# Optimization experiments

Measured on AMD Instinct MI355X. Metric: run time of the kernel, lower is better.

## Reference

```python
import jax, jax.numpy as jnp
import numpy as np
import math

DIM = 1024
NUM_HEADS = 16
HEAD_DIM = DIM // NUM_HEADS
MAX_SEQ_LEN = 2048


def setup_inputs() -> dict:
    key = jax.random.key(0)
    ks = jax.random.split(key, 10)
    B, S = 4, 2048
    std = 1.0 / math.sqrt(DIM)
    inp = {
        "x": jax.random.normal(ks[0], (B, S, DIM), dtype=jnp.float32),
        "key_padding_mask": jnp.zeros((B, S), dtype=jnp.bool_),
        "q_w": jax.random.uniform(ks[1], (DIM, DIM), minval=-std, maxval=std),
        "q_b": jax.random.uniform(ks[2], (DIM,), minval=-std, maxval=std),
        "k_w": jax.random.uniform(ks[3], (DIM, DIM), minval=-std, maxval=std),
        "k_b": jax.random.uniform(ks[4], (DIM,), minval=-std, maxval=std),
        "v_w": jax.random.uniform(ks[5], (DIM, DIM), minval=-std, maxval=std),
        "v_b": jax.random.uniform(ks[6], (DIM,), minval=-std, maxval=std),
        "o_w": jax.random.uniform(ks[7], (DIM, DIM), minval=-std, maxval=std),
        "o_b": jax.random.uniform(ks[8], (DIM,), minval=-std, maxval=std),
    }
    return inp


def _rope_tables(seq_len):
    # freqs over half the head dim, per the RotaryPositionalEmbedding module
    half = HEAD_DIM // 2
    freqs = 1.0 / (10000.0 ** (jnp.arange(0, HEAD_DIM, 2, dtype=jnp.float32) / HEAD_DIM))
    pos = jnp.arange(seq_len, dtype=jnp.float32)
    ang = jnp.outer(pos, freqs)  # [S, half]
    return jnp.cos(ang)[:, :half], jnp.sin(ang)[:, :half]


def _apply_rope(t, cos, sin):
    # t: [B, H, S, D]; rotate first/second halves (non-interleaved variant)
    half = HEAD_DIM // 2
    left, right = t[..., :half], t[..., half:]
    return jnp.concatenate([left * cos - right * sin,
                            left * sin + right * cos], axis=-1)


def reference(x, key_padding_mask, q_w, q_b, k_w, k_b, v_w, v_b, o_w, o_b):
    B, S, _ = x.shape
    scale = HEAD_DIM ** -0.5

    def proj(w, b):
        y = jnp.einsum('bsd,ed->bse', x, w) + b  # torch Linear: x @ W^T + b
        return y.reshape(B, S, NUM_HEADS, HEAD_DIM).transpose(0, 2, 1, 3)

    q = proj(q_w, q_b)  # [B, H, S, D]
    k = proj(k_w, k_b)
    v = proj(v_w, v_b)

    cos, sin = _rope_tables(S)  # [S, half], broadcast over B,H
    q = _apply_rope(q, cos, sin)
    k = _apply_rope(k, cos, sin)

    scores = jnp.einsum('bhqd,bhkd->bhqk', q, k) * scale
    scores = jnp.where(key_padding_mask[:, None, None, :], -1e9, scores)
    weights = jax.nn.softmax(scores, axis=-1)  # dropout p=0.0 -> identity
    out = jnp.einsum('bhqk,bhkd->bhqd', weights, v)
    out = out.transpose(0, 2, 1, 3).reshape(B, S, DIM)
    return jnp.einsum('bsd,ed->bse', out, o_w) + o_b
```

## Files before the change

kernel.cpp:

```cpp
#include <hip/hip_runtime.h>
#include <stdint.h>

#define SEQ   2048
#define BATCH 4
#define NH    16
#define HD    64
#define DIMN  1024
#define MROWS (BATCH*SEQ)

typedef __attribute__((ext_vector_type(8))) short          bf16x8;
typedef __attribute__((ext_vector_type(8))) unsigned short ushort8;
typedef __attribute__((ext_vector_type(4))) float          f32x4;

static __device__ __forceinline__ unsigned short f2bf(float f) {
    unsigned int u = __builtin_bit_cast(unsigned int, f);
    u += 0x7fffu + ((u >> 16) & 1u);
    return (unsigned short)(u >> 16);
}
static __device__ __forceinline__ unsigned int pack2bf(float lo, float hi) {
    unsigned int a = __builtin_bit_cast(unsigned int, lo) + 0x8000u;
    unsigned int b = __builtin_bit_cast(unsigned int, hi) + 0x8000u;
    return __builtin_amdgcn_perm(b, a, 0x07060302u);
}
static __device__ __forceinline__ unsigned int pack2bf_trunc(float lo, float hi) {
    return __builtin_amdgcn_perm(__builtin_bit_cast(unsigned int, hi),
                                 __builtin_bit_cast(unsigned int, lo), 0x07060302u);
}

__global__ __launch_bounds__(256) void prologue_kernel(
        const float* __restrict__ x,
        const float* __restrict__ qw, const float* __restrict__ kw,
        const float* __restrict__ vw, const float* __restrict__ ow,
        unsigned short* __restrict__ xb,
        unsigned short* __restrict__ wq, unsigned short* __restrict__ wk,
        unsigned short* __restrict__ wv, unsigned short* __restrict__ wo,
        float* __restrict__ cosT, float* __restrict__ sinT,
        const unsigned char* __restrict__ mask, unsigned long long* __restrict__ m64) {
    const int bx = blockIdx.x, tid = threadIdx.x;
    if (bx < 4096 + 2048) {
        const float* s; unsigned short* d; int i;
        if (bx < 4096) { s = x; d = xb; i = bx * 2048 + tid * 8; }
        else {
            int wb = bx - 4096;
            int wsel = wb >> 9;
            s = wsel == 0 ? qw : (wsel == 1 ? kw : (wsel == 2 ? vw : ow));
            d = wsel == 0 ? wq : (wsel == 1 ? wk : (wsel == 2 ? wv : wo));
            i = (wb & 511) * 2048 + tid * 8;
        }
        float4 a = *(const float4*)(s + i);
        float4 b = *(const float4*)(s + i + 4);
        ushort8 o;
        o[0]=f2bf(a.x); o[1]=f2bf(a.y); o[2]=f2bf(a.z); o[3]=f2bf(a.w);
        o[4]=f2bf(b.x); o[5]=f2bf(b.y); o[6]=f2bf(b.z); o[7]=f2bf(b.w);
        *(ushort8*)(d + i) = o;
    } else if (bx < 6400) {
        int idx = (bx - 6144) * 256 + tid;
        int s = idx >> 5, j = idx & 31;
        float t = (float)(2 * j) / 64.0f;
        float freq = 1.0f / powf(10000.0f, t);
        float ang  = (float)s * freq;
        cosT[idx] = cosf(ang);
        sinT[idx] = sinf(ang);
    } else {
        if (tid < 128) {
            int b = tid >> 5, kt = tid & 31;
            const unsigned char* p = mask + b * SEQ + kt * 64;
            unsigned long long v = 0;
            for (int j = 0; j < 64; j++) v |= (unsigned long long)(p[j] != 0) << j;
            m64[tid] = v;
        }
    }
}

__global__ __launch_bounds__(256) void gemm_qkvt(const unsigned short* __restrict__ X,
        const unsigned short* __restrict__ Wq, const unsigned short* __restrict__ Wk,
        const unsigned short* __restrict__ Wv,
        const float* __restrict__ bq, const float* __restrict__ bk, const float* __restrict__ bv,
        unsigned short* __restrict__ Qo, unsigned short* __restrict__ Ko, unsigned short* __restrict__ Vto,
        const float* __restrict__ cosT, const float* __restrict__ sinT) {
    __shared__ __align__(16) unsigned short As0[128 * 32];
    __shared__ __align__(16) unsigned short Bs0[128 * 32];
    __shared__ __align__(16) unsigned short As1[128 * 32];
    __shared__ __align__(16) unsigned short Bs1[128 * 32];
    const int which = blockIdx.x >> 3;
    const int tid  = threadIdx.x;
    const int wid  = tid >> 6, lane = tid & 63;
    const int quad = lane >> 4, l15 = lane & 15;
    const int wm   = wid >> 1,  wn  = wid & 1;

    const unsigned short *Ag, *Bg;
    int m0, n0;
    if (which < 2) {
        m0 = blockIdx.y * 128;
        n0 = (blockIdx.x & 7) * 128;
        Ag = X;  Bg = which == 0 ? Wq : Wk;
    } else {
        m0 = (blockIdx.x & 7) * 128;
        n0 = blockIdx.y * 128;
        Ag = Wv; Bg = X;
    }

    f32x4 acc[4][4];
#pragma unroll
    for (int i = 0; i < 4; i++)
#pragma unroll
        for (int j = 0; j < 4; j++) acc[i][j] = (f32x4)0.0f;

    const int rb = wid * 32 + (lane >> 2);
    const int cb = (((lane & 3) ^ ((lane >> 3) & 3)) * 8);
    const int rq = (quad ^ ((l15 >> 1) & 3)) * 8;

#define GSTAGE(BA, BB, KK) do {                                                             \
    _Pragma("unroll")                                                                       \
    for (int i_ = 0; i_ < 2; i_++) {                                                        \
        const unsigned short* ga_ = Ag + (size_t)(m0 + rb + i_ * 16) * DIMN + (KK) + cb;    \
        __builtin_amdgcn_global_load_lds((const __attribute__((address_space(1))) void*)ga_,\
            (__attribute__((address_space(3))) void*)&BA[(wid * 32 + i_ * 16) * 32], 16, 0, 0);\
        const unsigned short* gb_ = Bg + (size_t)(n0 + rb + i_ * 16) * DIMN + (KK) + cb;    \
        __builtin_amdgcn_global_load_lds((const __attribute__((address_space(1))) void*)gb_,\
            (__attribute__((address_space(3))) void*)&BB[(wid * 32 + i_ * 16) * 32], 16, 0, 0);\
    } } while (0)

#define GCOMP(BA, BB) do {                                                                  \
    bf16x8 af_[4], bf_[4];                                                                  \
    _Pragma("unroll")                                                                       \
    for (int f_ = 0; f_ < 4; f_++) af_[f_] = *(const bf16x8*)&BA[(wm * 64 + f_ * 16 + l15) * 32 + rq]; \
    _Pragma("unroll")                                                                       \
    for (int f_ = 0; f_ < 4; f_++) bf_[f_] = *(const bf16x8*)&BB[(wn * 64 + f_ * 16 + l15) * 32 + rq]; \
    _Pragma("unroll")                                                                       \
    for (int fm_ = 0; fm_ < 4; fm_++)                                                       \
        _Pragma("unroll")                                                                   \
        for (int fn_ = 0; fn_ < 4; fn_++)                                                   \
            acc[fm_][fn_] = __builtin_amdgcn_mfma_f32_16x16x32_bf16(af_[fm_], bf_[fn_], acc[fm_][fn_], 0, 0, 0); \
    } while (0)

    GSTAGE(As0, Bs0, 0);
    for (int k0 = 0; k0 < DIMN; k0 += 64) {
        __syncthreads();
        GSTAGE(As1, Bs1, k0 + 32);
        GCOMP(As0, Bs0);
        __syncthreads();
        if (k0 + 64 < DIMN) GSTAGE(As0, Bs0, k0 + 64);
        GCOMP(As1, Bs1);
    }

    if (which < 2) {
        const float* bias   = which == 0 ? bq : bk;
        unsigned short* Out = which == 0 ? Qo : Ko;
        const float scale = which == 0 ? 0.18033688011112042f : 1.0f;
        float bv4[4];
#pragma unroll
        for (int fn = 0; fn < 4; fn++) bv4[fn] = bias[n0 + wn * 64 + fn * 16 + l15];
        const int h = (n0 >> 6) + wn;
#pragma unroll
        for (int fm = 0; fm < 4; fm++)
#pragma unroll
            for (int r = 0; r < 4; r++) {
                int mrow = m0 + wm * 64 + fm * 16 + quad * 4 + r;
                int b = mrow >> 11, s = mrow & (SEQ - 1);
                unsigned short* orow = Out + ((size_t)(b * NH + h) * SEQ + s) * HD;
                float v0 = (acc[fm][0][r] + bv4[0]) * scale;
                float v1 = (acc[fm][1][r] + bv4[1]) * scale;
                float v2 = (acc[fm][2][r] + bv4[2]) * scale;
                float v3 = (acc[fm][3][r] + bv4[3]) * scale;
                int d0 = l15, d1 = 16 + l15;
                float c0 = cosT[s * 32 + d0], s0 = sinT[s * 32 + d0];
                float c1 = cosT[s * 32 + d1], s1 = sinT[s * 32 + d1];
                orow[d0]      = f2bf(v0 * c0 - v2 * s0);
                orow[d0 + 32] = f2bf(v0 * s0 + v2 * c0);
                orow[d1]      = f2bf(v1 * c1 - v3 * s1);
                orow[d1 + 32] = f2bf(v1 * s1 + v3 * c1);
            }
    } else {
        float4 bb[4];
#pragma unroll
        for (int fm = 0; fm < 4; fm++)
            bb[fm] = *(const float4*)&bv[m0 + wm * 64 + fm * 16 + quad * 4];
        const int b     = n0 >> 11;
        const int sbase = (n0 & (SEQ - 1)) + wn * 64 + l15;
#pragma unroll
        for (int fm = 0; fm < 4; fm++)
#pragma unroll
            for (int r = 0; r < 4; r++) {
                int e = m0 + wm * 64 + fm * 16 + quad * 4 + r;
                float bval = r == 0 ? bb[fm].x : (r == 1 ? bb[fm].y : (r == 2 ? bb[fm].z : bb[fm].w));
                unsigned short* row = Vto + ((size_t)(b * NH + (e >> 6)) * HD + (e & 63)) * SEQ + sbase;
#pragma unroll
                for (int fn = 0; fn < 4; fn++)
                    row[fn * 16] = f2bf(acc[fm][fn][r] + bval);
            }
    }
#undef GSTAGE
#undef GCOMP
}

__global__ __launch_bounds__(256) void gemm_bt(const unsigned short* __restrict__ A,
                                               const unsigned short* __restrict__ W,
                                               const float* __restrict__ bias,
                                               float* __restrict__ out) {
    __shared__ __align__(16) unsigned short As0[128 * 32];
    __shared__ __align__(16) unsigned short Bs0[128 * 32];
    __shared__ __align__(16) unsigned short As1[128 * 32];
    __shared__ __align__(16) unsigned short Bs1[128 * 32];
    const int tid  = threadIdx.x;
    const int wid  = tid >> 6, lane = tid & 63;
    const int quad = lane >> 4, l15 = lane & 15;
    const int wm   = wid >> 1,  wn  = wid & 1;
    const int m0   = blockIdx.y * 128, n0 = blockIdx.x * 128;

    f32x4 acc[4][4];
#pragma unroll
    for (int i = 0; i < 4; i++)
#pragma unroll
        for (int j = 0; j < 4; j++) acc[i][j] = (f32x4)0.0f;

    const int rb = wid * 32 + (lane >> 2);
    const int cb = (((lane & 3) ^ ((lane >> 3) & 3)) * 8);
    const int rq = (quad ^ ((l15 >> 1) & 3)) * 8;

#define GSTAGE(BA, BB, KK) do {                                                             \
    _Pragma("unroll")                                                                       \
    for (int i_ = 0; i_ < 2; i_++) {                                                        \
        const unsigned short* ga_ = A + (size_t)(m0 + rb + i_ * 16) * DIMN + (KK) + cb;     \
        __builtin_amdgcn_global_load_lds((const __attribute__((address_space(1))) void*)ga_,\
            (__attribute__((address_space(3))) void*)&BA[(wid * 32 + i_ * 16) * 32], 16, 0, 0);\
        const unsigned short* gb_ = W + (size_t)(n0 + rb + i_ * 16) * DIMN + (KK) + cb;     \
        __builtin_amdgcn_global_load_lds((const __attribute__((address_space(1))) void*)gb_,\
            (__attribute__((address_space(3))) void*)&BB[(wid * 32 + i_ * 16) * 32], 16, 0, 0);\
    } } while (0)

#define GCOMP(BA, BB) do {                                                                  \
    bf16x8 af_[4], bf_[4];                                                                  \
    _Pragma("unroll")                                                                       \
    for (int f_ = 0; f_ < 4; f_++) af_[f_] = *(const bf16x8*)&BA[(wm * 64 + f_ * 16 + l15) * 32 + rq]; \
    _Pragma("unroll")                                                                       \
    for (int f_ = 0; f_ < 4; f_++) bf_[f_] = *(const bf16x8*)&BB[(wn * 64 + f_ * 16 + l15) * 32 + rq]; \
    _Pragma("unroll")                                                                       \
    for (int fm_ = 0; fm_ < 4; fm_++)                                                       \
        _Pragma("unroll")                                                                   \
        for (int fn_ = 0; fn_ < 4; fn_++)                                                   \
            acc[fm_][fn_] = __builtin_amdgcn_mfma_f32_16x16x32_bf16(af_[fm_], bf_[fn_], acc[fm_][fn_], 0, 0, 0); \
    } while (0)

    GSTAGE(As0, Bs0, 0);
    for (int k0 = 0; k0 < DIMN; k0 += 64) {
        __syncthreads();
        GSTAGE(As1, Bs1, k0 + 32);
        GCOMP(As0, Bs0);
        __syncthreads();
        if (k0 + 64 < DIMN) GSTAGE(As0, Bs0, k0 + 64);
        GCOMP(As1, Bs1);
    }

    float bv4[4];
#pragma unroll
    for (int fn = 0; fn < 4; fn++) bv4[fn] = bias[n0 + wn * 64 + fn * 16 + l15];
#pragma unroll
    for (int fm = 0; fm < 4; fm++)
#pragma unroll
        for (int r = 0; r < 4; r++) {
            int mrow = m0 + wm * 64 + fm * 16 + quad * 4 + r;
            float* orow = out + (size_t)mrow * DIMN + n0 + wn * 64;
#pragma unroll
            for (int fn = 0; fn < 4; fn++) orow[fn * 16 + l15] = acc[fm][fn][r] + bv4[fn];
        }
#undef GSTAGE
#undef GCOMP
}

#define PSTRIDE 36
__global__ __launch_bounds__(256, 4) void attn_kernel(const unsigned short* __restrict__ Q,
                                                      const unsigned short* __restrict__ K,
                                                      const unsigned short* __restrict__ Vt,
                                                      const unsigned long long* __restrict__ M64,
                                                      unsigned short* __restrict__ Ob) {
    __shared__ __align__(16) unsigned short Ks[2][8 * 512];
    __shared__ __align__(16) unsigned short Vs[2][8 * 512];
    __shared__ __align__(16) unsigned short Ps[4 * 16 * PSTRIDE];

    const int tid  = threadIdx.x;
    const int wid  = tid >> 6, lane = tid & 63;
    const int quad = lane >> 4, l15 = lane & 15;
    const int bid = blockIdx.x;
    const int bh  = (bid & 7) * 8 + (bid >> 7);
    const int qt  = (bid >> 3) & 15;
    const int b = bh >> 4, h = bh & 15;
    const int q0 = qt * 128;

    bf16x8 qf[2][2];
#pragma unroll
    for (int n = 0; n < 2; n++) {
        const int qs = q0 + wid * 32 + n * 16 + l15;
#pragma unroll
        for (int dk = 0; dk < 2; dk++)
            qf[n][dk] = __builtin_bit_cast(bf16x8,
                *(const uint4*)&Q[((size_t)bh * SEQ + qs) * HD + dk * 32 + quad * 8]);
    }

    f32x4 Oa[4][2];
#pragma unroll
    for (int i = 0; i < 4; i++)
#pragma unroll
        for (int n = 0; n < 2; n++) Oa[i][n] = (f32x4)0.0f;
    float ls[2] = {0.0f, 0.0f};

    unsigned short* Pw = &Ps[wid * 16 * PSTRIDE];
    const unsigned long long* Mrow = M64 + b * (SEQ / 64);

    const int s0 = wid * 2, s1 = s0 + 1;
    const unsigned short* Kg = K + (size_t)bh * SEQ * HD;
    const unsigned short* Vg = Vt + (size_t)bh * HD * SEQ;
    const unsigned short* gk0 = Kg + (size_t)((s0 >> 1) * 16 + l15) * HD + (s0 & 1) * 32 + quad * 8;
    const unsigned short* gk1 = Kg + (size_t)((s1 >> 1) * 16 + l15) * HD + (s1 & 1) * 32 + quad * 8;
    const unsigned short* gv0 = Vg + (size_t)((s0 >> 1) * 16 + l15) * SEQ + (s0 & 1) * 32 + quad * 8;
    const unsigned short* gv1 = Vg + (size_t)((s1 >> 1) * 16 + l15) * SEQ + (s1 & 1) * 32 + quad * 8;

#define ASTAGE(K0, KSB, VSB) do {                                                        \
    __builtin_amdgcn_global_load_lds(                                                    \
        (const __attribute__((address_space(1))) void*)(gk0 + (size_t)(K0) * HD),        \
        (__attribute__((address_space(3))) void*)&KSB[s0 * 512], 16, 0, 0);              \
    __builtin_amdgcn_global_load_lds(                                                    \
        (const __attribute__((address_space(1))) void*)(gk1 + (size_t)(K0) * HD),        \
        (__attribute__((address_space(3))) void*)&KSB[s1 * 512], 16, 0, 0);              \
    __builtin_amdgcn_global_load_lds(                                                    \
        (const __attribute__((address_space(1))) void*)(gv0 + (K0)),                     \
        (__attribute__((address_space(3))) void*)&VSB[s0 * 512], 16, 0, 0);              \
    __builtin_amdgcn_global_load_lds(                                                    \
        (const __attribute__((address_space(1))) void*)(gv1 + (K0)),                     \
        (__attribute__((address_space(3))) void*)&VSB[s1 * 512], 16, 0, 0);              \
    } while (0)

    ASTAGE(0, Ks[0], Vs[0]);
    for (int kt = 0; kt < SEQ / 64; kt++) {
        unsigned long long mb = Mrow[kt];
        __syncthreads();
        const unsigned short* Kc = Ks[kt & 1];
        const unsigned short* Vc = Vs[kt & 1];
        if (kt + 1 < SEQ / 64) ASTAGE((kt + 1) * 64, Ks[(kt + 1) & 1], Vs[(kt + 1) & 1]);

#pragma unroll
        for (int h2 = 0; h2 < 2; h2++) {
            bf16x8 kf[2][2];
#pragma unroll
            for (int f2 = 0; f2 < 2; f2++)
#pragma unroll
                for (int dk = 0; dk < 2; dk++)
                    kf[f2][dk] = *(const bf16x8*)&Kc[(((h2 * 2 + f2) << 1) + dk) * 512 + lane * 8];
            bf16x8 vf[4];
#pragma unroll
            for (int df = 0; df < 4; df++)
                vf[df] = *(const bf16x8*)&Vc[((df << 1) + h2) * 512 + lane * 8];

            f32x4 st[2][2];
            __builtin_amdgcn_s_setprio(1);
#pragma unroll
            for (int f2 = 0; f2 < 2; f2++)
#pragma unroll
                for (int n = 0; n < 2; n++) {
                    st[f2][n] = __builtin_amdgcn_mfma_f32_16x16x32_bf16(kf[f2][0], qf[n][0], (f32x4)0.0f, 0, 0, 0);
                    st[f2][n] = __builtin_amdgcn_mfma_f32_16x16x32_bf16(kf[f2][1], qf[n][1], st[f2][n], 0, 0, 0);
                }
            __builtin_amdgcn_s_setprio(0);

            unsigned int mh = (unsigned int)(mb >> (h2 * 32));
            if (mh) {
#pragma unroll
                for (int f2 = 0; f2 < 2; f2++)
#pragma unroll
                    for (int n = 0; n < 2; n++)
#pragma unroll
                        for (int r = 0; r < 4; r++) {
                            int kk = f2 * 16 + quad * 4 + r;
                            if ((mh >> kk) & 1u) st[f2][n][r] = -1e9f;
                        }
            }

#pragma unroll
            for (int n = 0; n < 2; n++) {
#pragma unroll
                for (int f2 = 0; f2 < 2; f2++) {
                    float p0 = __builtin_amdgcn_exp2f(st[f2][n][0]);
                    float p1 = __builtin_amdgcn_exp2f(st[f2][n][1]);
                    float p2 = __builtin_amdgcn_exp2f(st[f2][n][2]);
                    float p3 = __builtin_amdgcn_exp2f(st[f2][n][3]);
                    ls[n] += (p0 + p1) + (p2 + p3);
                    uint2 w;
                    w.x = pack2bf_trunc(p0, p1);
                    w.y = pack2bf_trunc(p2, p3);
                    *(uint2*)&Pw[l15 * PSTRIDE + f2 * 16 + quad * 4] = w;
                }
                uint2 plo = *(const uint2*)&Pw[l15 * PSTRIDE + quad * 8];
                uint2 phi = *(const uint2*)&Pw[l15 * PSTRIDE + quad * 8 + 4];
                uint4 pw4;
                pw4.x = plo.x; pw4.y = plo.y; pw4.z = phi.x; pw4.w = phi.y;
                bf16x8 pf = __builtin_bit_cast(bf16x8, pw4);
                __builtin_amdgcn_s_setprio(1);
#pragma unroll
                for (int df = 0; df < 4; df++)
                    Oa[df][n] = __builtin_amdgcn_mfma_f32_16x16x32_bf16(vf[df], pf, Oa[df][n], 0, 0, 0);
                __builtin_amdgcn_s_setprio(0);
            }
        }
    }
#undef ASTAGE

    float linv[2];
#pragma unroll
    for (int n = 0; n < 2; n++) {
        float l = ls[n];
        l += __shfl_xor(l, 16);
        l += __shfl_xor(l, 32);
        linv[n] = 1.0f / l;
    }

#pragma unroll
    for (int n = 0; n < 2; n++) {
        int s = q0 + wid * 32 + n * 16 + l15;
        unsigned short* orow = Ob + ((size_t)b * SEQ + s) * DIMN + h * HD + quad * 4;
#pragma unroll
        for (int df = 0; df < 4; df++) {
            uint2 w;
            w.x = pack2bf(Oa[df][n][0] * linv[n], Oa[df][n][1] * linv[n]);
            w.y = pack2bf(Oa[df][n][2] * linv[n], Oa[df][n][3] * linv[n]);
            *(uint2*)&orow[df * 16] = w;
        }
    }
}

extern "C" void kernel_launch(void* const* d_in, const int* in_sizes, int n_in,
                              void* d_out, int out_size, void* d_ws, size_t ws_size,
                              hipStream_t stream) {
    (void)in_sizes; (void)n_in; (void)out_size; (void)ws_size;
    const float* x  = (const float*)d_in[0];
    const unsigned char* mask = (const unsigned char*)d_in[1];
    const float* q_w = (const float*)d_in[2];
    const float* q_b = (const float*)d_in[3];
    const float* k_w = (const float*)d_in[4];
    const float* k_b = (const float*)d_in[5];
    const float* v_w = (const float*)d_in[6];
    const float* v_b = (const float*)d_in[7];
    const float* o_w = (const float*)d_in[8];
    const float* o_b = (const float*)d_in[9];
    float* out = (float*)d_out;

    char* w = (char*)d_ws;
    unsigned short* xb = (unsigned short*)w;
    unsigned short* wq = (unsigned short*)(w + (16u << 20));
    unsigned short* wk = wq + (1u << 20);
    unsigned short* wv = wk + (1u << 20);
    unsigned short* wo = wv + (1u << 20);
    float* cosT = (float*)(w + (24u << 20));
    float* sinT = cosT + SEQ * 32;
    unsigned long long* m64 = (unsigned long long*)(w + (24u << 20) + (1u << 19));
    unsigned short* Qb  = (unsigned short*)(w + (25u << 20));
    unsigned short* Kb  = Qb + (8u << 20);
    unsigned short* Vtb = Kb + (8u << 20);
    unsigned short* Ob  = xb;

    prologue_kernel<<<dim3(6401), 256, 0, stream>>>(x, q_w, k_w, v_w, o_w,
                                                    xb, wq, wk, wv, wo,
                                                    cosT, sinT, mask, m64);

    gemm_qkvt<<<dim3(24, 64), 256, 0, stream>>>(xb, wq, wk, wv, q_b, k_b, v_b,
                                                Qb, Kb, Vtb, cosT, sinT);

    attn_kernel<<<dim3(1024), 256, 0, stream>>>(Qb, Kb, Vtb, m64, Ob);

    gemm_bt<<<dim3(DIMN / 128, MROWS / 128), 256, 0, stream>>>(Ob, wo, o_b, out);
}
```

Baseline: 285.9 us.

## Load attention K/V fragments directly from global into registers, dropping LDS staging

The attention kernel no longer stages K and V tiles through double-buffered shared memory with async global-to-LDS copies and a per-tile barrier. Each wave now reads its K and V MFMA fragments straight from global memory into registers, and prefetches the next K fragment in software while the current one is used. This removes the LDS footprint and the block-wide synchronisation. In exchange, every wave fetches the same K/V data on its own, raising cache and global traffic, and the final prefetch reads past the end of the current head's K rows.

```diff
diff --git a/kernel.cpp b/kernel.cpp
--- a/kernel.cpp
+++ b/kernel.cpp
@@ -274,8 +274,6 @@
                                                       const unsigned short* __restrict__ Vt,
                                                       const unsigned long long* __restrict__ M64,
                                                       unsigned short* __restrict__ Ob) {
-    __shared__ __align__(16) unsigned short Ks[2][8 * 512];
-    __shared__ __align__(16) unsigned short Vs[2][8 * 512];
     __shared__ __align__(16) unsigned short Ps[4 * 16 * PSTRIDE];
 
     const int tid  = threadIdx.x;
@@ -307,49 +305,31 @@
     unsigned short* Pw = &Ps[wid * 16 * PSTRIDE];
     const unsigned long long* Mrow = M64 + b * (SEQ / 64);
 
-    const int s0 = wid * 2, s1 = s0 + 1;
     const unsigned short* Kg = K + (size_t)bh * SEQ * HD;
     const unsigned short* Vg = Vt + (size_t)bh * HD * SEQ;
-    const unsigned short* gk0 = Kg + (size_t)((s0 >> 1) * 16 + l15) * HD + (s0 & 1) * 32 + quad * 8;
-    const unsigned short* gk1 = Kg + (size_t)((s1 >> 1) * 16 + l15) * HD + (s1 & 1) * 32 + quad * 8;
-    const unsigned short* gv0 = Vg + (size_t)((s0 >> 1) * 16 + l15) * SEQ + (s0 & 1) * 32 + quad * 8;
-    const unsigned short* gv1 = Vg + (size_t)((s1 >> 1) * 16 + l15) * SEQ + (s1 & 1) * 32 + quad * 8;
-
-#define ASTAGE(K0, KSB, VSB) do {                                                        \
-    __builtin_amdgcn_global_load_lds(                                                    \
-        (const __attribute__((address_space(1))) void*)(gk0 + (size_t)(K0) * HD),        \
-        (__attribute__((address_space(3))) void*)&KSB[s0 * 512], 16, 0, 0);              \
-    __builtin_amdgcn_global_load_lds(                                                    \
-        (const __attribute__((address_space(1))) void*)(gk1 + (size_t)(K0) * HD),        \
-        (__attribute__((address_space(3))) void*)&KSB[s1 * 512], 16, 0, 0);              \
-    __builtin_amdgcn_global_load_lds(                                                    \
-        (const __attribute__((address_space(1))) void*)(gv0 + (K0)),                     \
-        (__attribute__((address_space(3))) void*)&VSB[s0 * 512], 16, 0, 0);              \
-    __builtin_amdgcn_global_load_lds(                                                    \
-        (const __attribute__((address_space(1))) void*)(gv1 + (K0)),                     \
-        (__attribute__((address_space(3))) void*)&VSB[s1 * 512], 16, 0, 0);              \
-    } while (0)
-
-    ASTAGE(0, Ks[0], Vs[0]);
+
+    const unsigned short* pKn = Kg + (size_t)l15 * HD + quad * 8;
+    const unsigned short* pVm = Vg + (size_t)l15 * SEQ + quad * 8;
+
+    bf16x8 kf[2][2];
+#pragma unroll
+    for (int f2 = 0; f2 < 2; f2++)
+#pragma unroll
+        for (int dk = 0; dk < 2; dk++)
+            kf[f2][dk] = __builtin_bit_cast(bf16x8,
+                *(const uint4*)(pKn + f2 * 16 * HD + dk * 32));
+    pKn += 32 * HD;
+
     for (int kt = 0; kt < SEQ / 64; kt++) {
         unsigned long long mb = Mrow[kt];
-        __syncthreads();
-        const unsigned short* Kc = Ks[kt & 1];
-        const unsigned short* Vc = Vs[kt & 1];
-        if (kt + 1 < SEQ / 64) ASTAGE((kt + 1) * 64, Ks[(kt + 1) & 1], Vs[(kt + 1) & 1]);
-
 #pragma unroll
         for (int h2 = 0; h2 < 2; h2++) {
-            bf16x8 kf[2][2];
-#pragma unroll
-            for (int f2 = 0; f2 < 2; f2++)
-#pragma unroll
-                for (int dk = 0; dk < 2; dk++)
-                    kf[f2][dk] = *(const bf16x8*)&Kc[(((h2 * 2 + f2) << 1) + dk) * 512 + lane * 8];
             bf16x8 vf[4];
 #pragma unroll
             for (int df = 0; df < 4; df++)
-                vf[df] = *(const bf16x8*)&Vc[((df << 1) + h2) * 512 + lane * 8];
+                vf[df] = __builtin_bit_cast(bf16x8,
+                    *(const uint4*)(pVm + (size_t)df * 16 * SEQ));
+            pVm += 32;
 
             f32x4 st[2][2];
             __builtin_amdgcn_s_setprio(1);
@@ -361,6 +341,14 @@
                     st[f2][n] = __builtin_amdgcn_mfma_f32_16x16x32_bf16(kf[f2][1], qf[n][1], st[f2][n], 0, 0, 0);
                 }
             __builtin_amdgcn_s_setprio(0);
+
+#pragma unroll
+            for (int f2 = 0; f2 < 2; f2++)
+#pragma unroll
+                for (int dk = 0; dk < 2; dk++)
+                    kf[f2][dk] = __builtin_bit_cast(bf16x8,
+                        *(const uint4*)(pKn + f2 * 16 * HD + dk * 32));
+            pKn += 32 * HD;
 
             unsigned int mh = (unsigned int)(mb >> (h2 * 32));
             if (mh) {
@@ -402,7 +390,6 @@
             }
         }
     }
-#undef ASTAGE
 
     float linv[2];
 #pragma unroll
```

Result: slower. 466.1 us (+63.0%).
